# Kernel tuning notes

Hardware: AMD Instinct MI355X
Metric: run time of the kernel (lower is better)

The kernel has to match this reference:

```python
import jax, jax.numpy as jnp
import numpy as np

BS, SEQ, DK = 4, 4096, 128

def setup_inputs() -> dict:
    key = jax.random.key(0)
    kq, kk, kv = jax.random.split(key, 3)
    q = jax.random.normal(kq, (BS, SEQ, DK), dtype=jnp.float32)
    k = jax.random.normal(kk, (BS, SEQ, DK), dtype=jnp.float32)
    v = jax.random.normal(kv, (BS, SEQ, DK), dtype=jnp.float32)
    return {"q": q, "k": k, "v": v}

def reference(q, k, v):
    d_k = q.shape[-1]
    # scores: [bs, s_q, s_k]
    scaled = jnp.einsum('bqd,bkd->bqk', q, k) / jnp.sqrt(jnp.asarray(d_k, q.dtype))
    # NOTE: original torch code applies softmax over dim=1 (query axis), faithfully reproduced here.
    attn = jax.nn.softmax(scaled, axis=1)
    return jnp.einsum('bqk,bkd->bqd', attn, v)
```

## Files before the change

### kernel.cpp

```cpp
#include <hip/hip_runtime.h>
#include <hip/hip_bf16.h>

#define BS  4
#define SEQ 4096
#define DK  128

#define C1_SCALE (1.4426950408889634f / 11.313708498984761f)

typedef __attribute__((ext_vector_type(8))) short bf16x8;
typedef __attribute__((ext_vector_type(4))) float f32x4;
typedef __attribute__((ext_vector_type(16))) float f32x16;
typedef unsigned short ushort_t;

__device__ inline unsigned pk_bf16(float a, float b) {
    __hip_bfloat162 h = __float22bfloat162_rn(make_float2(a, b));
    union { __hip_bfloat162 h2; unsigned u; } cv;
    cv.h2 = h;
    return cv.u;
}

__device__ inline bf16x8 pk8(float4 a, float4 b) {
    union { bf16x8 v; unsigned u[4]; } r;
    r.u[0] = pk_bf16(a.x, a.y);
    r.u[1] = pk_bf16(a.z, a.w);
    r.u[2] = pk_bf16(b.x, b.y);
    r.u[3] = pk_bf16(b.z, b.w);
    return r.v;
}

__device__ inline void gld_lds16(const ushort_t* g, ushort_t* l) {
    __builtin_amdgcn_global_load_lds(
        (const __attribute__((address_space(1))) unsigned int*)g,
        (__attribute__((address_space(3))) unsigned int*)l,
        16, 0, 0);
}

__device__ inline void bar_fence() {
    __builtin_amdgcn_s_barrier();
    asm volatile("" ::: "memory");
}

__device__ inline void pl32_swap(unsigned &x, unsigned &y) {
    asm volatile("v_permlane32_swap_b32 %0, %1" : "+v"(x), "+v"(y));
}

__global__ __launch_bounds__(256) void cast_qk_sw(
    const float* __restrict__ Q, const float* __restrict__ K,
    ushort_t* __restrict__ Qb, ushort_t* __restrict__ Kb)
{
    const int g = blockIdx.x * 256 + threadIdx.x;
    const int q = g >> 4, ap = g & 15;
    const int a = ap ^ (q & 15);
    const float* src = Q + (size_t)q * DK + a * 8;
    float4 x = *(const float4*)src, y = *(const float4*)(src + 4);
    x.x *= C1_SCALE; x.y *= C1_SCALE; x.z *= C1_SCALE; x.w *= C1_SCALE;
    y.x *= C1_SCALE; y.y *= C1_SCALE; y.z *= C1_SCALE; y.w *= C1_SCALE;
    *(bf16x8*)(Qb + (size_t)g * 8) = pk8(x, y);
    src = K + (size_t)q * DK + a * 8;
    float4 x2 = *(const float4*)src, y2 = *(const float4*)(src + 4);
    *(bf16x8*)(Kb + (size_t)g * 8) = pk8(x2, y2);
}

__global__ __launch_bounds__(256) void sdpa_lsum(
    const ushort_t* __restrict__ Qb, const ushort_t* __restrict__ Kb,
    float* __restrict__ lp)
{
    __shared__ ushort_t Qs[3][4096];

    const int kt = blockIdx.x, qs = blockIdx.y, b = blockIdx.z;
    const int tid = threadIdx.x;
    const int w = tid >> 6, lane = tid & 63, ln = lane & 15, quad = lane >> 4;

    bf16x8 ka[2][4];
#pragma unroll
    for (int mt = 0; mt < 2; ++mt)
#pragma unroll
        for (int c = 0; c < 4; ++c)
            ka[mt][c] = *(const bf16x8*)(Kb +
                ((size_t)(b * SEQ) + kt * 128 + w * 32 + mt * 16 + ln) * DK +
                (((c * 4 + quad) ^ ln) * 8));

    float ls[2][4] = {};
    const ushort_t* qtb = Qb + ((size_t)(b * SEQ + qs * 512)) * DK;

#define A_DMA(BUF, I)                                                          \
    {                                                                          \
        _Pragma("unroll")                                                      \
        for (int j = 0; j < 2; ++j)                                            \
            gld_lds16(qtb + (size_t)(I) * 4096 + (j * 256 + tid) * 8,          \
                      &Qs[BUF][(j * 256 + w * 64) * 8]);                       \
    }

#define A_CMP(BUF)                                                             \
    {                                                                          \
        bf16x8 qf[2][4];                                                       \
        _Pragma("unroll")                                                      \
        for (int nt = 0; nt < 2; ++nt)                                         \
            _Pragma("unroll")                                                  \
            for (int c = 0; c < 4; ++c)                                        \
                qf[nt][c] = *(const bf16x8*)&Qs[BUF][(nt * 16 + ln) * 128 +    \
                                    (((c * 4 + quad) ^ ln) * 8)];              \
        _Pragma("unroll")                                                      \
        for (int mt = 0; mt < 2; ++mt)                                         \
            _Pragma("unroll")                                                  \
            for (int nt = 0; nt < 2; ++nt) {                                   \
                f32x4 s = {0.f, 0.f, 0.f, 0.f};                                \
                __builtin_amdgcn_s_setprio(1);                                 \
                _Pragma("unroll")                                              \
                for (int c = 0; c < 4; ++c)                                    \
                    s = __builtin_amdgcn_mfma_f32_16x16x32_bf16(               \
                        ka[mt][c], qf[nt][c], s, 0, 0, 0);                     \
                __builtin_amdgcn_s_setprio(0);                                 \
                _Pragma("unroll")                                              \
                for (int r = 0; r < 4; ++r)                                    \
                    ls[mt][r] += __builtin_amdgcn_exp2f(s[r]);                 \
            }                                                                  \
    }

    A_DMA(0, 0)
    A_DMA(1, 1)
    for (int t = 0; t < 15; ++t) {
        asm volatile("s_waitcnt vmcnt(2) lgkmcnt(0)" ::: "memory");
        bar_fence();
        if (t < 14) A_DMA((t + 2) % 3, t + 2)
        A_CMP(t % 3)
    }
    asm volatile("s_waitcnt vmcnt(0) lgkmcnt(0)" ::: "memory");
    bar_fence();
    A_CMP(0)
#undef A_DMA
#undef A_CMP

#pragma unroll
    for (int mt = 0; mt < 2; ++mt)
#pragma unroll
        for (int r = 0; r < 4; ++r) {
            float vv = ls[mt][r];
            vv += __shfl_xor(vv, 1);
            vv += __shfl_xor(vv, 2);
            vv += __shfl_xor(vv, 4);
            vv += __shfl_xor(vv, 8);
            ls[mt][r] = vv;
        }
    if (ln < 8) {
        int k = kt * 128 + w * 32 + (ln >> 2) * 16 + quad * 4 + (ln & 3);
        lp[((size_t)(qs * BS + b)) * SEQ + k] = ls[ln >> 2][ln & 3];
    }
}

__global__ __launch_bounds__(256) void vb_transpose(
    const float* __restrict__ V, const float* __restrict__ lp,
    ushort_t* __restrict__ VbT)
{
    __shared__ float Vl[64][132];
    __shared__ float Wl[64];

    const int kt = blockIdx.x, b = blockIdx.y;
    const int tid = threadIdx.x;
    const int k0 = kt * 64;
    {
        int r = tid >> 2, sg = tid & 3;
        const float* src = V + ((size_t)(b * SEQ) + k0 + r) * DK + sg * 32;
#pragma unroll
        for (int i = 0; i < 8; ++i)
            *(float4*)&Vl[r][sg * 32 + i * 4] = *(const float4*)(src + i * 4);
    }
    if (tid < 64) {
        float s = 0.f;
#pragma unroll
        for (int qs = 0; qs < 8; ++qs)
            s += lp[((size_t)(qs * BS + b)) * SEQ + k0 + tid];
        Wl[tid] = 1.0f / s;
    }
    __syncthreads();

    const int d = tid >> 1, kh = tid & 1;
    unsigned u[16];
#pragma unroll
    for (int j = 0; j < 16; ++j) {
        int row = kh * 32 + j * 2;
        u[j] = pk_bf16(Vl[row][d] * Wl[row], Vl[row + 1][d] * Wl[row + 1]);
    }
    ushort_t* dst = VbT + ((size_t)(b * DK) + d) * SEQ + k0 + kh * 32;
#pragma unroll
    for (int i = 0; i < 4; ++i) {
        uint4 t4; t4.x = u[i*4]; t4.y = u[i*4+1]; t4.z = u[i*4+2]; t4.w = u[i*4+3];
        *(uint4*)(dst + i * 8) = t4;
    }
}

__global__ __launch_bounds__(256, 2) void sdpa_out(
    const ushort_t* __restrict__ Qb, const ushort_t* __restrict__ Kb,
    const ushort_t* __restrict__ VbT,
    float* __restrict__ Op, float* __restrict__ O, int use_partial)
{
    __shared__ ushort_t Kt[2][64 * 128];
    __shared__ ushort_t Vt[2][128 * 64];

    const int g  = blockIdx.x;
    const int qt = blockIdx.y;
    const int ks = g >> 2, b = g & 3;
    const int tid = threadIdx.x;
    const int w = tid >> 6, lane = tid & 63;
    const int l31 = lane & 31, hi = lane >> 5;
    const int vdn = tid >> 3, van = tid & 7;

    const int qrow = qt * 128 + w * 32 + l31;
    const ushort_t* qb = Qb + ((size_t)(b * SEQ) + qrow) * DK;
    bf16x8 qa[8];
#pragma unroll
    for (int m = 0; m < 8; ++m)
        qa[m] = *(const bf16x8*)(qb + (((2 * m + hi) ^ (qrow & 15)) * 8));

    f32x16 acc[4];
#pragma unroll
    for (int i = 0; i < 4; ++i)
#pragma unroll
        for (int r = 0; r < 16; ++r) acc[i][r] = 0.f;

    const ushort_t* ksrc = Kb + ((size_t)(b * SEQ) + ks * 1024) * DK;
    const ushort_t* vsrc = VbT + ((size_t)(b * DK)) * SEQ + ks * 1024;

#define DMA_KV(BUF, T)                                                         \
    {                                                                          \
        _Pragma("unroll")                                                      \
        for (int j = 0; j < 4; ++j)                                            \
            gld_lds16(ksrc + (size_t)(T) * 64 * DK + (j * 256 + tid) * 8,      \
                      &Kt[BUF][(j * 256 + w * 64) * 8]);                       \
        _Pragma("unroll")                                                      \
        for (int j = 0; j < 4; ++j)                                            \
            gld_lds16(vsrc + (size_t)(j * 32 + vdn) * SEQ + (T) * 64 +         \
                          ((van ^ (vdn & 7)) * 8),                             \
                      &Vt[BUF][(j * 256 + w * 64) * 8]);                       \
    }

#define SUBTILE(BUF, S)                                                        \
    {                                                                          \
        bf16x8 kf[8];                                                          \
        _Pragma("unroll")                                                      \
        for (int m = 0; m < 8; ++m)                                            \
            kf[m] = *(const bf16x8*)&Kt[BUF][((S) * 32 + l31) * 128 +          \
                        (((2 * m + hi) ^ (l31 & 15)) * 8)];                    \
        f32x16 pA, pB;                                                         \
        _Pragma("unroll")                                                      \
        for (int r = 0; r < 16; ++r) { pA[r] = 0.f; pB[r] = 0.f; }             \
        __builtin_amdgcn_s_setprio(1);                                         \
        _Pragma("unroll")                                                      \
        for (int m = 0; m < 4; ++m)                                            \
            pA = __builtin_amdgcn_mfma_f32_32x32x16_bf16(kf[m], qa[m], pA, 0, 0, 0); \
        _Pragma("unroll")                                                      \
        for (int m = 0; m < 4; ++m)                                            \
            pB = __builtin_amdgcn_mfma_f32_32x32x16_bf16(kf[m + 4], qa[m + 4], pB, 0, 0, 0); \
        __builtin_amdgcn_s_setprio(0);                                         \
        unsigned wv[8];                                                        \
        _Pragma("unroll")                                                      \
        for (int j = 0; j < 8; ++j) {                                          \
            float e0 = __builtin_amdgcn_exp2f(pA[2 * j]     + pB[2 * j]);      \
            float e1 = __builtin_amdgcn_exp2f(pA[2 * j + 1] + pB[2 * j + 1]);  \
            wv[j] = pk_bf16(e0, e1);                                           \
        }                                                                      \
        pl32_swap(wv[0], wv[2]); pl32_swap(wv[1], wv[3]);                      \
        pl32_swap(wv[4], wv[6]); pl32_swap(wv[5], wv[7]);                      \
        bf16x8 pa0, pa1;                                                       \
        { union { unsigned u[4]; bf16x8 v; } c;                                \
          c.u[0] = wv[0]; c.u[1] = wv[1]; c.u[2] = wv[2]; c.u[3] = wv[3];      \
          pa0 = c.v;                                                           \
          c.u[0] = wv[4]; c.u[1] = wv[5]; c.u[2] = wv[6]; c.u[3] = wv[7];      \
          pa1 = c.v; }                                                         \
        _Pragma("unroll")                                                      \
        for (int dt = 0; dt < 4; ++dt) {                                       \
            bf16x8 v0 = *(const bf16x8*)&Vt[BUF][(dt * 32 + l31) * 64 +        \
                            ((((S) * 4 + 0 + hi) ^ (l31 & 7)) * 8)];           \
            bf16x8 v1 = *(const bf16x8*)&Vt[BUF][(dt * 32 + l31) * 64 +        \
                            ((((S) * 4 + 2 + hi) ^ (l31 & 7)) * 8)];           \
            __builtin_amdgcn_s_setprio(1);                                     \
            acc[dt] = __builtin_amdgcn_mfma_f32_32x32x16_bf16(v0, pa0, acc[dt], 0, 0, 0); \
            acc[dt] = __builtin_amdgcn_mfma_f32_32x32x16_bf16(v1, pa1, acc[dt], 0, 0, 0); \
            __builtin_amdgcn_s_setprio(0);                                     \
        }                                                                      \
    }

    DMA_KV(0, 0)
    DMA_KV(1, 1)

    for (int t = 0; t < 16; ++t) {
        if (t < 15) asm volatile("s_waitcnt vmcnt(8)" ::: "memory");
        else        asm volatile("s_waitcnt vmcnt(0)" ::: "memory");
        bar_fence();
        SUBTILE(t & 1, 0)
        SUBTILE(t & 1, 1)
        bar_fence();
        if (t < 14) DMA_KV(t & 1, t + 2)
    }
#undef DMA_KV
#undef SUBTILE

    if (use_partial) {
        float* dst = Op + (size_t)ks * ((size_t)BS * SEQ * DK) +
                     ((size_t)(b * SEQ) + qrow) * DK;
#pragma unroll
        for (int dt = 0; dt < 4; ++dt)
#pragma unroll
            for (int gg = 0; gg < 4; ++gg) {
                float4 v4;
                v4.x = acc[dt][gg * 4 + 0];
                v4.y = acc[dt][gg * 4 + 1];
                v4.z = acc[dt][gg * 4 + 2];
                v4.w = acc[dt][gg * 4 + 3];
                *(float4*)(dst + dt * 32 + gg * 8 + hi * 4) = v4;
            }
    } else {
        float* dst = O + ((size_t)(b * SEQ) + qrow) * DK;
#pragma unroll
        for (int dt = 0; dt < 4; ++dt)
#pragma unroll
            for (int gg = 0; gg < 4; ++gg)
#pragma unroll
                for (int i = 0; i < 4; ++i)
                    atomicAdd(dst + dt * 32 + gg * 8 + hi * 4 + i,
                              acc[dt][gg * 4 + i]);
    }
}

__global__ __launch_bounds__(256) void reduce4(
    const float* __restrict__ Op, float* __restrict__ O)
{
    const size_t N = (size_t)BS * SEQ * DK;
    size_t i = ((size_t)blockIdx.x * 256 + threadIdx.x) * 4;
    float4 a0 = *(const float4*)(Op + i);
    float4 a1 = *(const float4*)(Op + N + i);
    float4 a2 = *(const float4*)(Op + 2 * N + i);
    float4 a3 = *(const float4*)(Op + 3 * N + i);
    float4 r;
    r.x = a0.x + a1.x + a2.x + a3.x;
    r.y = a0.y + a1.y + a2.y + a3.y;
    r.z = a0.z + a1.z + a2.z + a3.z;
    r.w = a0.w + a1.w + a2.w + a3.w;
    *(float4*)(O + i) = r;
}

extern "C" void kernel_launch(void* const* d_in, const int* in_sizes, int n_in,
                              void* d_out, int out_size, void* d_ws, size_t ws_size,
                              hipStream_t stream) {
    const float* q = (const float*)d_in[0];
    const float* k = (const float*)d_in[1];
    const float* v = (const float*)d_in[2];
    float* out = (float*)d_out;

    const size_t QKV = (size_t)BS * SEQ * DK;
    float*    lp  = (float*)d_ws;
    ushort_t* Qb  = (ushort_t*)((char*)d_ws + (1 << 20));
    ushort_t* Kb  = Qb + QKV;
    ushort_t* VbT = Kb + QKV;
    float*    Op  = (float*)(VbT + QKV);

    const size_t need_p = (1u << 20) + 3 * QKV * 2 + 4 * QKV * sizeof(float);

    cast_qk_sw<<<dim3(BS * SEQ * 16 / 256), 256, 0, stream>>>(q, k, Qb, Kb);
    sdpa_lsum  <<<dim3(32, 8, 4), 256, 0, stream>>>(Qb, Kb, lp);
    vb_transpose<<<dim3(64, 4),   256, 0, stream>>>(v, lp, VbT);

    if (ws_size >= need_p) {
        sdpa_out<<<dim3(16, 32), 256, 0, stream>>>(Qb, Kb, VbT, Op, out, 1);
        reduce4<<<dim3(BS * SEQ * DK / 4 / 256), 256, 0, stream>>>(Op, out);
    } else {
        hipMemsetAsync(out, 0, QKV * sizeof(float), stream);
        sdpa_out<<<dim3(16, 32), 256, 0, stream>>>(Qb, Kb, VbT, nullptr, out, 0);
    }
}
```

Baseline: 150.1 us.

## Double split factors for column-sum and output kernels to raise parallelism

The column-sum kernel now covers 256 query rows per block instead of 512, so its grid doubles. The output kernel splits the key axis 8 ways using 32-key tiles instead of 4 ways with 64-key tiles. It halves shared memory and asks for 4 blocks per CU, giving more workgroups and higher occupancy. In exchange the reduction now sums 8 partial buffers, which doubles the partial write and read traffic and the workspace it needs. Each block also does less work to hide pipeline latency.

```diff
diff --git a/kernel.cpp b/kernel.cpp
--- a/kernel.cpp
+++ b/kernel.cpp
@@ -81,7 +81,7 @@
                 (((c * 4 + quad) ^ ln) * 8));
 
     float ls[2][4] = {};
-    const ushort_t* qtb = Qb + ((size_t)(b * SEQ + qs * 512)) * DK;
+    const ushort_t* qtb = Qb + ((size_t)(b * SEQ + qs * 256)) * DK;
 
 #define A_DMA(BUF, I)                                                          \
     {                                                                          \
@@ -119,15 +119,15 @@
 
     A_DMA(0, 0)
     A_DMA(1, 1)
-    for (int t = 0; t < 15; ++t) {
+    for (int t = 0; t < 7; ++t) {
         asm volatile("s_waitcnt vmcnt(2) lgkmcnt(0)" ::: "memory");
         bar_fence();
-        if (t < 14) A_DMA((t + 2) % 3, t + 2)
+        if (t < 6) A_DMA((t + 2) % 3, t + 2)
         A_CMP(t % 3)
     }
     asm volatile("s_waitcnt vmcnt(0) lgkmcnt(0)" ::: "memory");
     bar_fence();
-    A_CMP(0)
+    A_CMP(1)
 #undef A_DMA
 #undef A_CMP
 
@@ -168,7 +168,7 @@
     if (tid < 64) {
         float s = 0.f;
 #pragma unroll
-        for (int qs = 0; qs < 8; ++qs)
+        for (int qs = 0; qs < 16; ++qs)
             s += lp[((size_t)(qs * BS + b)) * SEQ + k0 + tid];
         Wl[tid] = 1.0f / s;
     }
@@ -189,13 +189,13 @@
     }
 }
 
-__global__ __launch_bounds__(256, 2) void sdpa_out(
+__global__ __launch_bounds__(256, 4) void sdpa_out(
     const ushort_t* __restrict__ Qb, const ushort_t* __restrict__ Kb,
     const ushort_t* __restrict__ VbT,
     float* __restrict__ Op, float* __restrict__ O, int use_partial)
 {
-    __shared__ ushort_t Kt[2][64 * 128];
-    __shared__ ushort_t Vt[2][128 * 64];
+    __shared__ ushort_t Kt[2][32 * 128];
+    __shared__ ushort_t Vt[2][128 * 32];
 
     const int g  = blockIdx.x;
     const int qt = blockIdx.y;
@@ -203,7 +203,6 @@
     const int tid = threadIdx.x;
     const int w = tid >> 6, lane = tid & 63;
     const int l31 = lane & 31, hi = lane >> 5;
-    const int vdn = tid >> 3, van = tid & 7;
 
     const int qrow = qt * 128 + w * 32 + l31;
     const ushort_t* qb = Qb + ((size_t)(b * SEQ) + qrow) * DK;
@@ -218,28 +217,28 @@
 #pragma unroll
         for (int r = 0; r < 16; ++r) acc[i][r] = 0.f;
 
-    const ushort_t* ksrc = Kb + ((size_t)(b * SEQ) + ks * 1024) * DK;
-    const ushort_t* vsrc = VbT + ((size_t)(b * DK)) * SEQ + ks * 1024;
+    const ushort_t* ksrc = Kb + ((size_t)(b * SEQ) + ks * 512) * DK;
+    const ushort_t* vsrc = VbT + ((size_t)(b * DK)) * SEQ + ks * 512;
 
 #define DMA_KV(BUF, T)                                                         \
     {                                                                          \
         _Pragma("unroll")                                                      \
-        for (int j = 0; j < 4; ++j)                                            \
-            gld_lds16(ksrc + (size_t)(T) * 64 * DK + (j * 256 + tid) * 8,      \
+        for (int j = 0; j < 2; ++j)                                            \
+            gld_lds16(ksrc + (size_t)(T) * 32 * DK + (j * 256 + tid) * 8,      \
                       &Kt[BUF][(j * 256 + w * 64) * 8]);                       \
         _Pragma("unroll")                                                      \
-        for (int j = 0; j < 4; ++j)                                            \
-            gld_lds16(vsrc + (size_t)(j * 32 + vdn) * SEQ + (T) * 64 +         \
-                          ((van ^ (vdn & 7)) * 8),                             \
+        for (int j = 0; j < 2; ++j)                                            \
+            gld_lds16(vsrc + (size_t)(j * 64 + (tid >> 2)) * SEQ + (T) * 32 +  \
+                          (((tid & 3) ^ ((tid >> 2) & 3)) * 8),                \
                       &Vt[BUF][(j * 256 + w * 64) * 8]);                       \
     }
 
-#define SUBTILE(BUF, S)                                                        \
+#define SUBTILE(BUF)                                                           \
     {                                                                          \
         bf16x8 kf[8];                                                          \
         _Pragma("unroll")                                                      \
         for (int m = 0; m < 8; ++m)                                            \
-            kf[m] = *(const bf16x8*)&Kt[BUF][((S) * 32 + l31) * 128 +          \
+            kf[m] = *(const bf16x8*)&Kt[BUF][l31 * 128 +                       \
                         (((2 * m + hi) ^ (l31 & 15)) * 8)];                    \
         f32x16 pA, pB;                                                         \
         _Pragma("unroll")                                                      \
@@ -269,10 +268,10 @@
           pa1 = c.v; }                                                         \
         _Pragma("unroll")                                                      \
         for (int dt = 0; dt < 4; ++dt) {                                       \
-            bf16x8 v0 = *(const bf16x8*)&Vt[BUF][(dt * 32 + l31) * 64 +        \
-                            ((((S) * 4 + 0 + hi) ^ (l31 & 7)) * 8)];           \
-            bf16x8 v1 = *(const bf16x8*)&Vt[BUF][(dt * 32 + l31) * 64 +        \
-                            ((((S) * 4 + 2 + hi) ^ (l31 & 7)) * 8)];           \
+            bf16x8 v0 = *(const bf16x8*)&Vt[BUF][(dt * 32 + l31) * 32 +        \
+                            (((0 + hi) ^ (l31 & 3)) * 8)];                     \
+            bf16x8 v1 = *(const bf16x8*)&Vt[BUF][(dt * 32 + l31) * 32 +        \
+                            (((2 + hi) ^ (l31 & 3)) * 8)];                     \
             __builtin_amdgcn_s_setprio(1);                                     \
             acc[dt] = __builtin_amdgcn_mfma_f32_32x32x16_bf16(v0, pa0, acc[dt], 0, 0, 0); \
             acc[dt] = __builtin_amdgcn_mfma_f32_32x32x16_bf16(v1, pa1, acc[dt], 0, 0, 0); \
@@ -284,11 +283,10 @@
     DMA_KV(1, 1)
 
     for (int t = 0; t < 16; ++t) {
-        if (t < 15) asm volatile("s_waitcnt vmcnt(8)" ::: "memory");
+        if (t < 15) asm volatile("s_waitcnt vmcnt(4)" ::: "memory");
         else        asm volatile("s_waitcnt vmcnt(0)" ::: "memory");
         bar_fence();
-        SUBTILE(t & 1, 0)
-        SUBTILE(t & 1, 1)
+        SUBTILE(t & 1)
         bar_fence();
         if (t < 14) DMA_KV(t & 1, t + 2)
     }
@@ -322,20 +320,17 @@
     }
 }
 
-__global__ __launch_bounds__(256) void reduce4(
+__global__ __launch_bounds__(256) void reduce8(
     const float* __restrict__ Op, float* __restrict__ O)
 {
     const size_t N = (size_t)BS * SEQ * DK;
     size_t i = ((size_t)blockIdx.x * 256 + threadIdx.x) * 4;
-    float4 a0 = *(const float4*)(Op + i);
-    float4 a1 = *(const float4*)(Op + N + i);
-    float4 a2 = *(const float4*)(Op + 2 * N + i);
-    float4 a3 = *(const float4*)(Op + 3 * N + i);
-    float4 r;
-    r.x = a0.x + a1.x + a2.x + a3.x;
-    r.y = a0.y + a1.y + a2.y + a3.y;
-    r.z = a0.z + a1.z + a2.z + a3.z;
-    r.w = a0.w + a1.w + a2.w + a3.w;
+    float4 r = *(const float4*)(Op + i);
+#pragma unroll
+    for (int s = 1; s < 8; ++s) {
+        float4 a = *(const float4*)(Op + (size_t)s * N + i);
+        r.x += a.x; r.y += a.y; r.z += a.z; r.w += a.w;
+    }
     *(float4*)(O + i) = r;
 }
 
@@ -354,17 +349,17 @@
     ushort_t* VbT = Kb + QKV;
     float*    Op  = (float*)(VbT + QKV);
 
-    const size_t need_p = (1u << 20) + 3 * QKV * 2 + 4 * QKV * sizeof(float);
+    const size_t need_p = (1u << 20) + 3 * QKV * 2 + 8 * QKV * sizeof(float);
 
     cast_qk_sw<<<dim3(BS * SEQ * 16 / 256), 256, 0, stream>>>(q, k, Qb, Kb);
-    sdpa_lsum  <<<dim3(32, 8, 4), 256, 0, stream>>>(Qb, Kb, lp);
-    vb_transpose<<<dim3(64, 4),   256, 0, stream>>>(v, lp, VbT);
+    sdpa_lsum  <<<dim3(32, 16, 4), 256, 0, stream>>>(Qb, Kb, lp);
+    vb_transpose<<<dim3(64, 4),    256, 0, stream>>>(v, lp, VbT);
 
     if (ws_size >= need_p) {
-        sdpa_out<<<dim3(16, 32), 256, 0, stream>>>(Qb, Kb, VbT, Op, out, 1);
-        reduce4<<<dim3(BS * SEQ * DK / 4 / 256), 256, 0, stream>>>(Op, out);
+        sdpa_out<<<dim3(32, 32), 256, 0, stream>>>(Qb, Kb, VbT, Op, out, 1);
+        reduce8<<<dim3(BS * SEQ * DK / 4 / 256), 256, 0, stream>>>(Op, out);
     } else {
         hipMemsetAsync(out, 0, QKV * sizeof(float), stream);
-        sdpa_out<<<dim3(16, 32), 256, 0, stream>>>(Qb, Kb, VbT, nullptr, out, 0);
-    }
-}
+        sdpa_out<<<dim3(32, 32), 256, 0, stream>>>(Qb, Kb, VbT, nullptr, out, 0);
+    }
+}
```

Measured after the change: 227.9 us. 1.52x slower.
